# Kernel tuning notes

Hardware: AMD Instinct MI355X
Metric: run time of the kernel (lower is better)

Reference implementation:

```python
import jax, jax.numpy as jnp
import numpy as np

B = 512
IN_F, HID, OUT_F = 342, 512, 311


def setup_inputs() -> dict:
    key = jax.random.key(0)
    ks = jax.random.split(key, 8)
    return {
        "p": jax.random.uniform(ks[0], (B,), dtype=jnp.float32),
        "x": jax.random.normal(ks[1], (B, IN_F), dtype=jnp.float32),
        "W0": jax.random.normal(ks[2], (4, IN_F, HID), dtype=jnp.float32) * 0.05,
        "b0": jax.random.normal(ks[3], (4, HID), dtype=jnp.float32) * 0.05,
        "W1": jax.random.normal(ks[4], (4, HID, HID), dtype=jnp.float32) * 0.05,
        "b1": jax.random.normal(ks[5], (4, HID), dtype=jnp.float32) * 0.05,
        "W2": jax.random.normal(ks[6], (4, HID, OUT_F), dtype=jnp.float32) * 0.05,
        "b2": jax.random.normal(ks[7], (4, OUT_F), dtype=jnp.float32) * 0.05,
    }


def _cubic(y0, y1, y2, y3, mu, mu2, mu3):
    # Catmull-Rom cubic interpolation (same coefficients as the torch module)
    return ((-0.5 * y0 + 1.5 * y1 - 1.5 * y2 + 0.5 * y3) * mu3
            + (y0 - 2.5 * y1 + 2.0 * y2 - 0.5 * y3) * mu2
            + (-0.5 * y0 + 0.5 * y2) * mu
            + y1)


def reference(p, x, W0, b0, W1, b1, W2, b2):
    p4 = p * 4.0
    pa = jnp.mod(p4, 1.0)                      # (B,) fractional phase
    i1 = p4.astype(jnp.int32) % 4              # (B,) control point indices
    i0 = (i1 - 1) % 4
    i2 = (i1 + 1) % 4
    i3 = (i1 + 2) % 4

    wa = pa[:, None, None]                     # (B,1,1) for weights
    wa2, wa3 = wa * wa, wa * wa * wa
    ba = pa[:, None]                           # (B,1) for biases
    ba2, ba3 = ba * ba, ba * ba * ba

    def interp_w(W):  # W: (4, din, dout) -> (B, din, dout)
        return _cubic(W[i0], W[i1], W[i2], W[i3], wa, wa2, wa3)

    def interp_b(b):  # b: (4, d) -> (B, d)
        return _cubic(b[i0], b[i1], b[i2], b[i3], ba, ba2, ba3)

    h = jax.nn.elu(jnp.einsum('bi,bio->bo', x, interp_w(W0)) + interp_b(b0))
    h = jax.nn.elu(jnp.einsum('bi,bio->bo', h, interp_w(W1)) + interp_b(b1))
    y = jnp.einsum('bi,bio->bo', h, interp_w(W2)) + interp_b(b2)
    return y
```

## Files before the change

### kernel.cpp

```cpp
#include <hip/hip_runtime.h>
#include <math.h>

typedef __bf16 bf16x8 __attribute__((ext_vector_type(8)));
typedef float f32x4 __attribute__((ext_vector_type(4)));

#define B_SZ 512
#define IN_F 342
#define HID  512
#define OUT_F 311
#define K0P  1536
#define K12  2048
#define N2P  320
#define SPLIT 4

__global__ __launch_bounds__(256) void setup_kernel(
    const float* __restrict__ p, const float* __restrict__ x,
    const float* __restrict__ W0, const float* __restrict__ W1,
    const float* __restrict__ W2, float* __restrict__ coef,
    __bf16* __restrict__ A0, __bf16* __restrict__ T0,
    __bf16* __restrict__ T1, __bf16* __restrict__ T2) {
  int bid = blockIdx.x;
  int tid = threadIdx.x;
  if (bid < B_SZ) {
    int b = bid;
    __shared__ float cf[4];
    if (tid == 0) {
      float p4 = p[b] * 4.0f;
      float mu = p4 - floorf(p4);
      int i1 = ((int)p4) & 3;
      float mu2 = mu * mu, mu3 = mu2 * mu;
      float c0 = -0.5f * mu3 + mu2 - 0.5f * mu;
      float c1 =  1.5f * mu3 - 2.5f * mu2 + 1.0f;
      float c2 = -1.5f * mu3 + 2.0f * mu2 + 0.5f * mu;
      float c3 =  0.5f * mu3 - 0.5f * mu2;
      cf[(i1 + 3) & 3] = c0;
      cf[i1]           = c1;
      cf[(i1 + 1) & 3] = c2;
      cf[(i1 + 2) & 3] = c3;
    }
    __syncthreads();
    if (tid < 4) coef[b * 4 + tid] = cf[tid];
    float c0 = cf[0], c1 = cf[1], c2 = cf[2], c3 = cf[3];
    const float* xr = x + (size_t)b * IN_F;
    __bf16* dst = A0 + (size_t)b * K0P;
    for (int i = tid; i < IN_F; i += 256) {
      float xv = xr[i];
      dst[i]            = (__bf16)(c0 * xv);
      dst[IN_F + i]     = (__bf16)(c1 * xv);
      dst[2 * IN_F + i] = (__bf16)(c2 * xv);
      dst[3 * IN_F + i] = (__bf16)(c3 * xv);
    }
    for (int k = 4 * IN_F + tid; k < K0P; k += 256) dst[k] = (__bf16)0.0f;
    return;
  }
  bid -= B_SZ;
  const float* W; __bf16* T; int K, N, Kp, tk, t;
  if (bid < 192)      { W = W0; T = T0; K = 1368; N = 512; Kp = K0P; t = bid;       tk = 24; }
  else if (bid < 448) { W = W1; T = T1; K = 2048; N = 512; Kp = K12; t = bid - 192; tk = 32; }
  else                { W = W2; T = T2; K = 2048; N = 311; Kp = K12; t = bid - 448; tk = 32; }
  int k0 = (t % tk) * 64, n0 = (t / tk) * 64;
  __shared__ __bf16 tile[64][72];
  int nl = tid & 63, n = n0 + nl;
#pragma unroll
  for (int r = 0; r < 16; ++r) {
    int kl = (tid >> 6) + r * 4;
    int k = k0 + kl;
    float v = (k < K && n < N) ? W[(size_t)k * N + n] : 0.0f;
    tile[nl][kl] = (__bf16)v;
  }
  __syncthreads();
  int row = tid >> 2, o0 = (tid & 3) * 2;
  bf16x8 v0 = *(const bf16x8*)&tile[row][o0 * 8];
  bf16x8 v1 = *(const bf16x8*)&tile[row][o0 * 8 + 8];
  __bf16* dst = T + (size_t)(n0 + row) * Kp + k0 + o0 * 8;
  *(bf16x8*)dst = v0;
  *(bf16x8*)(dst + 8) = v1;
}

__global__ __launch_bounds__(256) void gemm_splitk(
    const __bf16* __restrict__ A, const __bf16* __restrict__ BT,
    float* __restrict__ P, int Ka, int Np, int C) {
  constexpr int LDT = 72;
  __shared__ __bf16 Als[64 * LDT];
  __shared__ __bf16 Bls[64 * LDT];

  const int tid = threadIdx.x;
  const int l = tid & 63;
  const int wave = tid >> 6;
  const int wm = wave >> 1, wn = wave & 1;
  const int lr = l & 15, lk = l >> 4;
  const int m0 = blockIdx.y * 64;
  const int n0 = blockIdx.x * 64;
  const int kbase = blockIdx.z * C;
  const int T = C >> 6;

  const int ar = tid >> 2;
  const int ao = (tid & 3) * 2;

  const __bf16* Ap = A + (size_t)(m0 + ar) * Ka + kbase + ao * 8;
  const __bf16* Bp = BT + (size_t)(n0 + ar) * Ka + kbase + ao * 8;

  bf16x8 a0_, a1_, b0_, b1_;
  bf16x8 a2_, a3_, b2_, b3_;
  f32x4 acc[2][2] = {};

  auto load0 = [&](int t) {
    a0_ = *(const bf16x8*)&Ap[t * 64];
    a1_ = *(const bf16x8*)&Ap[t * 64 + 8];
    b0_ = *(const bf16x8*)&Bp[t * 64];
    b1_ = *(const bf16x8*)&Bp[t * 64 + 8];
  };
  auto load1 = [&](int t) {
    a2_ = *(const bf16x8*)&Ap[t * 64];
    a3_ = *(const bf16x8*)&Ap[t * 64 + 8];
    b2_ = *(const bf16x8*)&Bp[t * 64];
    b3_ = *(const bf16x8*)&Bp[t * 64 + 8];
  };
  auto store0 = [&]() {
    *(bf16x8*)&Als[ar * LDT + ao * 8] = a0_;
    *(bf16x8*)&Als[ar * LDT + ao * 8 + 8] = a1_;
    *(bf16x8*)&Bls[ar * LDT + ao * 8] = b0_;
    *(bf16x8*)&Bls[ar * LDT + ao * 8 + 8] = b1_;
  };
  auto store1 = [&]() {
    *(bf16x8*)&Als[ar * LDT + ao * 8] = a2_;
    *(bf16x8*)&Als[ar * LDT + ao * 8 + 8] = a3_;
    *(bf16x8*)&Bls[ar * LDT + ao * 8] = b2_;
    *(bf16x8*)&Bls[ar * LDT + ao * 8 + 8] = b3_;
  };
  auto compute = [&]() {
#pragma unroll
    for (int kk = 0; kk < 64; kk += 32) {
      bf16x8 af[2], bg[2];
#pragma unroll
      for (int i = 0; i < 2; ++i) {
        af[i] = *(const bf16x8*)&Als[(wm * 32 + i * 16 + lr) * LDT + kk + lk * 8];
        bg[i] = *(const bf16x8*)&Bls[(wn * 32 + i * 16 + lr) * LDT + kk + lk * 8];
      }
#pragma unroll
      for (int i = 0; i < 2; ++i)
#pragma unroll
        for (int j = 0; j < 2; ++j)
          acc[i][j] = __builtin_amdgcn_mfma_f32_16x16x32_bf16(af[i], bg[j],
                                                              acc[i][j], 0, 0, 0);
    }
  };

  load0(0);
  load1(1);
  for (int t = 0; t < T; t += 2) {
    __syncthreads();
    store0();
    __syncthreads();
    if (t + 2 < T) load0(t + 2);
    compute();
    __syncthreads();
    store1();
    __syncthreads();
    if (t + 3 < T) load1(t + 3);
    compute();
  }

  float* Pp = P + (size_t)blockIdx.z * B_SZ * Np;
#pragma unroll
  for (int i = 0; i < 2; ++i)
#pragma unroll
    for (int j = 0; j < 2; ++j) {
      int gn = n0 + wn * 32 + j * 16 + lr;
#pragma unroll
      for (int r = 0; r < 4; ++r) {
        int gm = m0 + wm * 32 + i * 16 + lk * 4 + r;
        Pp[(size_t)gm * Np + gn] = acc[i][j][r];
      }
    }
}

template <int EXPAND, int NP>
__global__ __launch_bounds__(256) void epilogue_kernel(
    const float* __restrict__ P, const float* __restrict__ bias,
    const float* __restrict__ coef, void* __restrict__ outv, int N) {
  int idx = blockIdx.x * 256 + threadIdx.x;
  int m = idx / NP, n = idx - m * NP;
  if (m >= B_SZ || n >= N) return;
  float v = P[idx] + P[idx + B_SZ * NP] + P[idx + 2 * B_SZ * NP] +
            P[idx + 3 * B_SZ * NP];
  f32x4 cf = *(const f32x4*)&coef[m * 4];
  v += cf[0] * bias[n] + cf[1] * bias[N + n] + cf[2] * bias[2 * N + n] +
       cf[3] * bias[3 * N + n];
  if (EXPAND) {
    v = (v > 0.0f) ? v : expm1f(v);
    __bf16* dst = (__bf16*)outv + (size_t)m * (4 * N) + n;
    dst[0]     = (__bf16)(cf[0] * v);
    dst[N]     = (__bf16)(cf[1] * v);
    dst[2 * N] = (__bf16)(cf[2] * v);
    dst[3 * N] = (__bf16)(cf[3] * v);
  } else {
    ((float*)outv)[(size_t)m * N + n] = v;
  }
}

extern "C" void kernel_launch(void* const* d_in, const int* in_sizes, int n_in,
                              void* d_out, int out_size, void* d_ws, size_t ws_size,
                              hipStream_t stream) {
  const float* p  = (const float*)d_in[0];
  const float* x  = (const float*)d_in[1];
  const float* W0 = (const float*)d_in[2];
  const float* b0 = (const float*)d_in[3];
  const float* W1 = (const float*)d_in[4];
  const float* b1 = (const float*)d_in[5];
  const float* W2 = (const float*)d_in[6];
  const float* b2 = (const float*)d_in[7];
  float* out = (float*)d_out;

  char* w = (char*)d_ws;
  float*  coef = (float*)w;                 w += 8192;
  __bf16* A0   = (__bf16*)w;                w += (size_t)B_SZ * K0P * 2;
  __bf16* A1   = (__bf16*)w;                w += (size_t)B_SZ * K12 * 2;
  __bf16* A2   = (__bf16*)w;                w += (size_t)B_SZ * K12 * 2;
  __bf16* WT0  = (__bf16*)w;                w += (size_t)HID * K0P * 2;
  __bf16* WT1  = (__bf16*)w;                w += (size_t)HID * K12 * 2;
  __bf16* WT2  = (__bf16*)w;                w += (size_t)N2P * K12 * 2;
  float*  P    = (float*)w;

  setup_kernel<<<B_SZ + 608, 256, 0, stream>>>(p, x, W0, W1, W2, coef, A0,
                                               WT0, WT1, WT2);

  gemm_splitk<<<dim3(8, 8, SPLIT), 256, 0, stream>>>(A0, WT0, P, K0P, HID, K0P / SPLIT);
  epilogue_kernel<1, HID><<<B_SZ * HID / 256, 256, 0, stream>>>(P, b0, coef, A1, HID);

  gemm_splitk<<<dim3(8, 8, SPLIT), 256, 0, stream>>>(A1, WT1, P, K12, HID, K12 / SPLIT);
  epilogue_kernel<1, HID><<<B_SZ * HID / 256, 256, 0, stream>>>(P, b1, coef, A2, HID);

  gemm_splitk<<<dim3(N2P / 64, 8, SPLIT), 256, 0, stream>>>(A2, WT2, P, K12, N2P, K12 / SPLIT);
  epilogue_kernel<0, N2P><<<B_SZ * N2P / 256, 256, 0, stream>>>(P, b2, coef, out, OUT_F);
}
```

Measured before the change: 42.03 us.

## Fuse bias, ELU and coefficient expansion into next GEMM's A-tile prologue

Removes the separate epilogue kernels and the bf16 A0/A1/A2 activation buffers. Each GEMM block now builds its whole A panel in LDS directly from x or from the previous layer's split-K partials, applying bias, ELU and the per-row spline coefficient for its K chunk. Layer 0 uses a 384-padded layout with split 2, and the weight pack is remapped to match. This cuts two launches and some global round trips, at the cost of redundant partial-sum and ELU work across N-blocks and a larger LDS footprint that may lower occupancy.

Result: slower. 88.97 us (+111.7%).

```diff
diff --git a/kernel.cpp b/kernel.cpp
--- a/kernel.cpp
+++ b/kernel.cpp
@@ -2,29 +2,25 @@
 #include <math.h>
 
 typedef __bf16 bf16x8 __attribute__((ext_vector_type(8)));
+typedef __bf16 bf16x4 __attribute__((ext_vector_type(4)));
 typedef float f32x4 __attribute__((ext_vector_type(4)));
 
 #define B_SZ 512
 #define IN_F 342
 #define HID  512
 #define OUT_F 311
+#define N2P  320
 #define K0P  1536
 #define K12  2048
-#define N2P  320
-#define SPLIT 4
 
 __global__ __launch_bounds__(256) void setup_kernel(
-    const float* __restrict__ p, const float* __restrict__ x,
-    const float* __restrict__ W0, const float* __restrict__ W1,
-    const float* __restrict__ W2, float* __restrict__ coef,
-    __bf16* __restrict__ A0, __bf16* __restrict__ T0,
+    const float* __restrict__ p, const float* __restrict__ W0,
+    const float* __restrict__ W1, const float* __restrict__ W2,
+    float* __restrict__ coef, __bf16* __restrict__ T0,
     __bf16* __restrict__ T1, __bf16* __restrict__ T2) {
-  int bid = blockIdx.x;
-  int tid = threadIdx.x;
-  if (bid < B_SZ) {
-    int b = bid;
-    __shared__ float cf[4];
-    if (tid == 0) {
+  int bid = blockIdx.x, tid = threadIdx.x;
+  if (bid == 608) {
+    for (int b = tid; b < B_SZ; b += 256) {
       float p4 = p[b] * 4.0f;
       float mu = p4 - floorf(p4);
       int i1 = ((int)p4) & 3;
@@ -33,39 +29,36 @@
       float c1 =  1.5f * mu3 - 2.5f * mu2 + 1.0f;
       float c2 = -1.5f * mu3 + 2.0f * mu2 + 0.5f * mu;
       float c3 =  0.5f * mu3 - 0.5f * mu2;
-      cf[(i1 + 3) & 3] = c0;
-      cf[i1]           = c1;
-      cf[(i1 + 1) & 3] = c2;
-      cf[(i1 + 2) & 3] = c3;
-    }
-    __syncthreads();
-    if (tid < 4) coef[b * 4 + tid] = cf[tid];
-    float c0 = cf[0], c1 = cf[1], c2 = cf[2], c3 = cf[3];
-    const float* xr = x + (size_t)b * IN_F;
-    __bf16* dst = A0 + (size_t)b * K0P;
-    for (int i = tid; i < IN_F; i += 256) {
-      float xv = xr[i];
-      dst[i]            = (__bf16)(c0 * xv);
-      dst[IN_F + i]     = (__bf16)(c1 * xv);
-      dst[2 * IN_F + i] = (__bf16)(c2 * xv);
-      dst[3 * IN_F + i] = (__bf16)(c3 * xv);
-    }
-    for (int k = 4 * IN_F + tid; k < K0P; k += 256) dst[k] = (__bf16)0.0f;
+      float arr[4];
+      arr[(i1 + 3) & 3] = c0;
+      arr[i1]           = c1;
+      arr[(i1 + 1) & 3] = c2;
+      arr[(i1 + 2) & 3] = c3;
+      coef[b * 4 + 0] = arr[0];
+      coef[b * 4 + 1] = arr[1];
+      coef[b * 4 + 2] = arr[2];
+      coef[b * 4 + 3] = arr[3];
+    }
     return;
   }
-  bid -= B_SZ;
-  const float* W; __bf16* T; int K, N, Kp, tk, t;
-  if (bid < 192)      { W = W0; T = T0; K = 1368; N = 512; Kp = K0P; t = bid;       tk = 24; }
-  else if (bid < 448) { W = W1; T = T1; K = 2048; N = 512; Kp = K12; t = bid - 192; tk = 32; }
-  else                { W = W2; T = T2; K = 2048; N = 311; Kp = K12; t = bid - 448; tk = 32; }
+  const float* W; __bf16* T; int N, Kp, tk, t, job;
+  if (bid < 192)      { W = W0; T = T0; N = 512; Kp = K0P; t = bid;       tk = 24; job = 0; }
+  else if (bid < 448) { W = W1; T = T1; N = 512; Kp = K12; t = bid - 192; tk = 32; job = 1; }
+  else                { W = W2; T = T2; N = 311; Kp = K12; t = bid - 448; tk = 32; job = 2; }
   int k0 = (t % tk) * 64, n0 = (t / tk) * 64;
-  __shared__ __bf16 tile[64][72];
+  __shared__ __bf16 tile[64][66];
   int nl = tid & 63, n = n0 + nl;
 #pragma unroll
   for (int r = 0; r < 16; ++r) {
     int kl = (tid >> 6) + r * 4;
     int k = k0 + kl;
-    float v = (k < K && n < N) ? W[(size_t)k * N + n] : 0.0f;
+    float v = 0.0f;
+    if (job == 0) {
+      int c = k / 384, i = k - c * 384;
+      if (i < IN_F && n < N) v = W[(size_t)(c * IN_F + i) * 512 + n];
+    } else {
+      if (n < N) v = W[(size_t)k * ((job == 2) ? OUT_F : HID) + n];
+    }
     tile[nl][kl] = (__bf16)v;
   }
   __syncthreads();
@@ -77,11 +70,21 @@
   *(bf16x8*)(dst + 8) = v1;
 }
 
-__global__ __launch_bounds__(256) void gemm_splitk(
-    const __bf16* __restrict__ A, const __bf16* __restrict__ BT,
-    float* __restrict__ P, int Ka, int Np, int C) {
+template <int LAYER>
+__global__ __launch_bounds__(256) void gemm_layer(
+    const float* __restrict__ src,
+    const __bf16* __restrict__ WT,
+    const float* __restrict__ biasPrev,
+    const float* __restrict__ coef,
+    float* __restrict__ Pout) {
+  constexpr int C   = (LAYER == 0) ? 768 : 512;
+  constexpr int T   = C / 64;
+  constexpr int LDA = (LAYER == 0) ? 776 : 520;
+  constexpr int KA  = (LAYER == 0) ? K0P : K12;
+  constexpr int NP  = (LAYER == 2) ? N2P : HID;
+  constexpr int PS  = (LAYER == 1) ? 2 : 4;
   constexpr int LDT = 72;
-  __shared__ __bf16 Als[64 * LDT];
+  __shared__ __bf16 Als[64 * LDA];
   __shared__ __bf16 Bls[64 * LDT];
 
   const int tid = threadIdx.x;
@@ -91,50 +94,39 @@
   const int lr = l & 15, lk = l >> 4;
   const int m0 = blockIdx.y * 64;
   const int n0 = blockIdx.x * 64;
-  const int kbase = blockIdx.z * C;
-  const int T = C >> 6;
+  const int zz = blockIdx.z;
 
   const int ar = tid >> 2;
   const int ao = (tid & 3) * 2;
-
-  const __bf16* Ap = A + (size_t)(m0 + ar) * Ka + kbase + ao * 8;
-  const __bf16* Bp = BT + (size_t)(n0 + ar) * Ka + kbase + ao * 8;
-
-  bf16x8 a0_, a1_, b0_, b1_;
-  bf16x8 a2_, a3_, b2_, b3_;
+  const __bf16* Bp = WT + (size_t)(n0 + ar) * KA + zz * C + ao * 8;
+
+  bf16x8 b0_, b1_;
+  bf16x8 b2_, b3_;
   f32x4 acc[2][2] = {};
 
   auto load0 = [&](int t) {
-    a0_ = *(const bf16x8*)&Ap[t * 64];
-    a1_ = *(const bf16x8*)&Ap[t * 64 + 8];
     b0_ = *(const bf16x8*)&Bp[t * 64];
     b1_ = *(const bf16x8*)&Bp[t * 64 + 8];
   };
   auto load1 = [&](int t) {
-    a2_ = *(const bf16x8*)&Ap[t * 64];
-    a3_ = *(const bf16x8*)&Ap[t * 64 + 8];
     b2_ = *(const bf16x8*)&Bp[t * 64];
     b3_ = *(const bf16x8*)&Bp[t * 64 + 8];
   };
   auto store0 = [&]() {
-    *(bf16x8*)&Als[ar * LDT + ao * 8] = a0_;
-    *(bf16x8*)&Als[ar * LDT + ao * 8 + 8] = a1_;
     *(bf16x8*)&Bls[ar * LDT + ao * 8] = b0_;
     *(bf16x8*)&Bls[ar * LDT + ao * 8 + 8] = b1_;
   };
   auto store1 = [&]() {
-    *(bf16x8*)&Als[ar * LDT + ao * 8] = a2_;
-    *(bf16x8*)&Als[ar * LDT + ao * 8 + 8] = a3_;
     *(bf16x8*)&Bls[ar * LDT + ao * 8] = b2_;
     *(bf16x8*)&Bls[ar * LDT + ao * 8 + 8] = b3_;
   };
-  auto compute = [&]() {
+  auto compute = [&](int t) {
 #pragma unroll
     for (int kk = 0; kk < 64; kk += 32) {
       bf16x8 af[2], bg[2];
 #pragma unroll
       for (int i = 0; i < 2; ++i) {
-        af[i] = *(const bf16x8*)&Als[(wm * 32 + i * 16 + lr) * LDT + kk + lk * 8];
+        af[i] = *(const bf16x8*)&Als[(wm * 32 + i * 16 + lr) * LDA + t * 64 + kk + lk * 8];
         bg[i] = *(const bf16x8*)&Bls[(wn * 32 + i * 16 + lr) * LDT + kk + lk * 8];
       }
 #pragma unroll
@@ -148,20 +140,73 @@
 
   load0(0);
   load1(1);
+
+  if (LAYER == 0) {
+    const int lane = tid & 63, grp = tid >> 6;
+    for (int r = grp; r < 64; r += 4) {
+      const f32x4 cf = *(const f32x4*)&coef[(m0 + r) * 4];
+      float s0 = zz ? cf[2] : cf[0];
+      float s1 = zz ? cf[3] : cf[1];
+      const float* xr = src + (size_t)(m0 + r) * IN_F;
+#pragma unroll
+      for (int j = 0; j < 6; ++j) {
+        int i = lane + j * 64;
+        if (i < IN_F) {
+          float xv = xr[i];
+          Als[r * LDA + i]       = (__bf16)(s0 * xv);
+          Als[r * LDA + 384 + i] = (__bf16)(s1 * xv);
+        }
+      }
+      if (lane < 384 - IN_F) {
+        Als[r * LDA + IN_F + lane]       = (__bf16)0.0f;
+        Als[r * LDA + 384 + IN_F + lane] = (__bf16)0.0f;
+      }
+    }
+  } else {
+    const int half = tid >> 7;
+    const int nn = (tid & 127) * 4;
+    const f32x4 bb0 = *(const f32x4*)&biasPrev[nn];
+    const f32x4 bb1 = *(const f32x4*)&biasPrev[HID + nn];
+    const f32x4 bb2 = *(const f32x4*)&biasPrev[2 * HID + nn];
+    const f32x4 bb3 = *(const f32x4*)&biasPrev[3 * HID + nn];
+    for (int r2 = 0; r2 < 64; r2 += 2) {
+      int r = r2 + half;
+      int gm = m0 + r;
+      f32x4 s = *(const f32x4*)&src[((size_t)0 * B_SZ + gm) * HID + nn];
+      s += *(const f32x4*)&src[((size_t)1 * B_SZ + gm) * HID + nn];
+      if (PS == 4) {
+        s += *(const f32x4*)&src[((size_t)2 * B_SZ + gm) * HID + nn];
+        s += *(const f32x4*)&src[((size_t)3 * B_SZ + gm) * HID + nn];
+      }
+      f32x4 cf = *(const f32x4*)&coef[gm * 4];
+      f32x4 v = s + cf[0] * bb0 + cf[1] * bb1 + cf[2] * bb2 + cf[3] * bb3;
+      float sc = (zz & 2) ? ((zz & 1) ? cf[3] : cf[2])
+                          : ((zz & 1) ? cf[1] : cf[0]);
+      bf16x4 o;
+#pragma unroll
+      for (int j = 0; j < 4; ++j) {
+        float e = v[j];
+        e = (e > 0.0f) ? e : expm1f(e);
+        o[j] = (__bf16)(sc * e);
+      }
+      *(bf16x4*)&Als[r * LDA + nn] = o;
+    }
+  }
+
   for (int t = 0; t < T; t += 2) {
     __syncthreads();
     store0();
     __syncthreads();
     if (t + 2 < T) load0(t + 2);
-    compute();
+    compute(t);
     __syncthreads();
     store1();
     __syncthreads();
     if (t + 3 < T) load1(t + 3);
-    compute();
-  }
-
-  float* Pp = P + (size_t)blockIdx.z * B_SZ * Np;
+    compute(t + 1);
+  }
+
+  float* Pp = Pout + (size_t)zz * B_SZ * NP;
 #pragma unroll
   for (int i = 0; i < 2; ++i)
 #pragma unroll
@@ -170,32 +215,24 @@
 #pragma unroll
       for (int r = 0; r < 4; ++r) {
         int gm = m0 + wm * 32 + i * 16 + lk * 4 + r;
-        Pp[(size_t)gm * Np + gn] = acc[i][j][r];
-      }
-    }
-}
-
-template <int EXPAND, int NP>
-__global__ __launch_bounds__(256) void epilogue_kernel(
-    const float* __restrict__ P, const float* __restrict__ bias,
-    const float* __restrict__ coef, void* __restrict__ outv, int N) {
-  int idx = blockIdx.x * 256 + threadIdx.x;
-  int m = idx / NP, n = idx - m * NP;
-  if (m >= B_SZ || n >= N) return;
-  float v = P[idx] + P[idx + B_SZ * NP] + P[idx + 2 * B_SZ * NP] +
-            P[idx + 3 * B_SZ * NP];
+        Pp[(size_t)gm * NP + gn] = acc[i][j][r];
+      }
+    }
+}
+
+__global__ __launch_bounds__(256) void final_epi(
+    const float* __restrict__ P3, const float* __restrict__ b2,
+    const float* __restrict__ coef, float* __restrict__ out) {
+  int m = blockIdx.x;
   f32x4 cf = *(const f32x4*)&coef[m * 4];
-  v += cf[0] * bias[n] + cf[1] * bias[N + n] + cf[2] * bias[2 * N + n] +
-       cf[3] * bias[3 * N + n];
-  if (EXPAND) {
-    v = (v > 0.0f) ? v : expm1f(v);
-    __bf16* dst = (__bf16*)outv + (size_t)m * (4 * N) + n;
-    dst[0]     = (__bf16)(cf[0] * v);
-    dst[N]     = (__bf16)(cf[1] * v);
-    dst[2 * N] = (__bf16)(cf[2] * v);
-    dst[3 * N] = (__bf16)(cf[3] * v);
-  } else {
-    ((float*)outv)[(size_t)m * N + n] = v;
+  for (int n = threadIdx.x; n < OUT_F; n += 256) {
+    float s = P3[((size_t)0 * B_SZ + m) * N2P + n] +
+              P3[((size_t)1 * B_SZ + m) * N2P + n] +
+              P3[((size_t)2 * B_SZ + m) * N2P + n] +
+              P3[((size_t)3 * B_SZ + m) * N2P + n];
+    float bi = cf[0] * b2[n] + cf[1] * b2[OUT_F + n] +
+               cf[2] * b2[2 * OUT_F + n] + cf[3] * b2[3 * OUT_F + n];
+    out[(size_t)m * OUT_F + n] = s + bi;
   }
 }
 
@@ -213,24 +250,18 @@
   float* out = (float*)d_out;
 
   char* w = (char*)d_ws;
-  float*  coef = (float*)w;                 w += 8192;
-  __bf16* A0   = (__bf16*)w;                w += (size_t)B_SZ * K0P * 2;
-  __bf16* A1   = (__bf16*)w;                w += (size_t)B_SZ * K12 * 2;
-  __bf16* A2   = (__bf16*)w;                w += (size_t)B_SZ * K12 * 2;
-  __bf16* WT0  = (__bf16*)w;                w += (size_t)HID * K0P * 2;
-  __bf16* WT1  = (__bf16*)w;                w += (size_t)HID * K12 * 2;
-  __bf16* WT2  = (__bf16*)w;                w += (size_t)N2P * K12 * 2;
-  float*  P    = (float*)w;
-
-  setup_kernel<<<B_SZ + 608, 256, 0, stream>>>(p, x, W0, W1, W2, coef, A0,
-                                               WT0, WT1, WT2);
-
-  gemm_splitk<<<dim3(8, 8, SPLIT), 256, 0, stream>>>(A0, WT0, P, K0P, HID, K0P / SPLIT);
-  epilogue_kernel<1, HID><<<B_SZ * HID / 256, 256, 0, stream>>>(P, b0, coef, A1, HID);
-
-  gemm_splitk<<<dim3(8, 8, SPLIT), 256, 0, stream>>>(A1, WT1, P, K12, HID, K12 / SPLIT);
-  epilogue_kernel<1, HID><<<B_SZ * HID / 256, 256, 0, stream>>>(P, b1, coef, A2, HID);
-
-  gemm_splitk<<<dim3(N2P / 64, 8, SPLIT), 256, 0, stream>>>(A2, WT2, P, K12, N2P, K12 / SPLIT);
-  epilogue_kernel<0, N2P><<<B_SZ * N2P / 256, 256, 0, stream>>>(P, b2, coef, out, OUT_F);
-}
+  float*  coef = (float*)w;   w += 8192;
+  __bf16* WT0  = (__bf16*)w;  w += (size_t)HID * K0P * 2;
+  __bf16* WT1  = (__bf16*)w;  w += (size_t)HID * K12 * 2;
+  __bf16* WT2  = (__bf16*)w;  w += (size_t)N2P * K12 * 2;
+  float*  P1   = (float*)w;   w += (size_t)2 * B_SZ * HID * 4;
+  float*  P2   = (float*)w;   w += (size_t)4 * B_SZ * HID * 4;
+  float*  P3   = (float*)w;   w += (size_t)4 * B_SZ * N2P * 4;
+
+  setup_kernel<<<609, 256, 0, stream>>>(p, W0, W1, W2, coef, WT0, WT1, WT2);
+
+  gemm_layer<0><<<dim3(8, 8, 2), 256, 0, stream>>>(x,  WT0, nullptr, coef, P1);
+  gemm_layer<1><<<dim3(8, 8, 4), 256, 0, stream>>>(P1, WT1, b0,      coef, P2);
+  gemm_layer<2><<<dim3(5, 8, 4), 256, 0, stream>>>(P2, WT2, b1,      coef, P3);
+  final_epi<<<B_SZ, 256, 0, stream>>>(P3, b2, coef, out);
+}
```
